# Performance work log

Measured on AMD Instinct MI355X. Metric: run time of the kernel, lower is better.

The kernel has to match this reference:

```python
import jax, jax.numpy as jnp
import numpy as np

N_NODES = 50000
N_EDGES = 800000
D_IN, D_LAT, D_EMB = 512, 256, 64
NEG_SLOPE = 0.2


def segment_softmax(logits, seg, num_segments):
    # numerically stable softmax over variable-size neighborhoods grouped by seg
    m = jax.ops.segment_max(logits, seg, num_segments=num_segments)
    e = jnp.exp(logits - m[seg])
    s = jax.ops.segment_sum(e, seg, num_segments=num_segments)
    return e / s[seg]


def setup_inputs() -> dict:
    key = jax.random.key(0)
    k = jax.random.split(key, 6)
    x = jax.random.normal(k[0], (N_NODES, D_IN), dtype=jnp.float32)
    graph_edges = jax.random.randint(k[1], (2, N_EDGES), 0, N_NODES, dtype=jnp.int32)
    # learned parameters (glorot-ish scaling)
    W1 = jax.random.normal(k[2], (D_IN, D_LAT), dtype=jnp.float32) / np.sqrt(D_IN)
    a1_src = jax.random.normal(k[3], (D_LAT,), dtype=jnp.float32) / np.sqrt(D_LAT)
    a1_dst = jax.random.normal(k[4], (D_LAT,), dtype=jnp.float32) / np.sqrt(D_LAT)
    W2 = jax.random.normal(k[5], (D_LAT, D_EMB), dtype=jnp.float32) / np.sqrt(D_LAT)
    return {"x": x, "W1": W1, "a1_src": a1_src, "a1_dst": a1_dst, "W2": W2,
            "graph_edges": graph_edges}


def reference(x, W1, a1_src, a1_dst, W2, graph_edges):
    src = graph_edges[0]  # message source j
    dst = graph_edges[1]  # aggregation target i
    n = x.shape[0]

    # --- encoder layer 1 (full GAT, heads=1, no bias, no self loops) ---
    h1 = x @ W1                                   # [N, D_LAT]
    als = h1 @ a1_src                             # [N] per-node src logits
    ald = h1 @ a1_dst                             # [N] per-node dst logits
    e1 = jax.nn.leaky_relu(als[src] + ald[dst], NEG_SLOPE)   # [E]
    alpha1 = segment_softmax(e1, dst, n)          # [E]
    agg1 = jax.ops.segment_sum(alpha1[:, None] * h1[src], dst, num_segments=n)
    inter = jax.nn.elu(agg1)                      # [N, D_LAT]

    # --- encoder layer 2 (compute_attention=False -> plain linear) ---
    emb = inter @ W2                              # [N, D_EMB]

    # --- decoder layer 1 (weights tied to W2^T, attention tied to layer1) ---
    h3 = emb @ W2.T                               # [N, D_LAT]
    # tied attention: reuse layer1's per-node logits (als, ald)
    e3 = jax.nn.leaky_relu(als[src] + ald[dst], NEG_SLOPE)
    alpha3 = segment_softmax(e3, dst, n)
    agg3 = jax.ops.segment_sum(alpha3[:, None] * h3[src], dst, num_segments=n)
    dec_inter = jax.nn.elu(agg3)                  # [N, D_LAT]

    # --- decoder layer 2 (compute_attention=False -> plain linear, W1^T) ---
    recon = dec_inter @ W1.T                      # [N, D_IN]
    return emb, recon
```

## Files before the change

### kernel.cpp

```cpp
#include <hip/hip_runtime.h>
#include <math.h>

#define N_NODES 50000
#define N_EDGES 800000
#define D_IN 512
#define D_LAT 256
#define D_EMB 64
#define NEG_SLOPE 0.2f

typedef __attribute__((ext_vector_type(8))) short bf16x8;
typedef __attribute__((ext_vector_type(8))) unsigned short u16x8;
typedef __attribute__((ext_vector_type(4))) float f32x4;

__device__ __forceinline__ ushort f2b(float f) {
  union { float f; unsigned u; } v; v.f = f;
  return (ushort)((v.u + 0x7fffu + ((v.u >> 16) & 1u)) >> 16);
}
__device__ __forceinline__ float b2f(ushort h) {
  union { unsigned u; float f; } v; v.u = ((unsigned)h) << 16;
  return v.f;
}

__device__ __forceinline__ float wave_reduce_sum(float v) {
#pragma unroll
  for (int off = 32; off > 0; off >>= 1) v += __shfl_xor(v, off, 64);
  return v;
}
__device__ __forceinline__ float wave_reduce_max(float v) {
#pragma unroll
  for (int off = 32; off > 0; off >>= 1) v = fmaxf(v, __shfl_xor(v, off, 64));
  return v;
}

template <int BM, int BN, int WR, int WC, int AF32, int WF32, int WBF16,
          int ELU>
__global__ __launch_bounds__(WR * WC * 64) void gemm_mfma(
    const void* __restrict__ Aptr, const ushort* __restrict__ B,
    float* __restrict__ Cf, ushort* __restrict__ Cb, int M, int N, int K) {
  constexpr int BK = 32;
  constexpr int WTM = BM / WR, WTN = BN / WC;
  constexpr int FM = WTM / 16, FN = WTN / 16;
  constexpr int NT = WR * WC * 64;
  constexpr int AIT = (BM * BK * 2) / (NT * 16);
  constexpr int BIT_ = (BN * BK * 2) / (NT * 16);
  __shared__ ushort As[BM][BK];
  __shared__ ushort Bs[BN][BK];
  const int tid = threadIdx.x, lane = tid & 63, wid = tid >> 6;
  const int wr = wid / WC, wc = wid % WC;
  const int bm = blockIdx.y * BM, bn = blockIdx.x * BN;
  f32x4 acc[FM][FN] = {};

  for (int k0 = 0; k0 < K; k0 += BK) {
    if constexpr (AF32) {
      const float* Af = (const float*)Aptr;
#pragma unroll
      for (int it = 0; it < AIT; ++it) {
        int off = it * (NT * 16) + tid * 16;
        int row = off >> 6;
        int ecol = (off & 63) >> 1;
        int grow = bm + row; grow = grow < M ? grow : (M - 1);
        const float* g = Af + (size_t)grow * K + k0 + ecol;
        float4 f0 = *(const float4*)g;
        float4 f1 = *(const float4*)(g + 4);
        u16x8 hb;
        hb[0] = f2b(f0.x); hb[1] = f2b(f0.y); hb[2] = f2b(f0.z); hb[3] = f2b(f0.w);
        hb[4] = f2b(f1.x); hb[5] = f2b(f1.y); hb[6] = f2b(f1.z); hb[7] = f2b(f1.w);
        *(u16x8*)((char*)&As[0][0] + off) = hb;
      }
    } else {
      const ushort* Ab = (const ushort*)Aptr;
#pragma unroll
      for (int it = 0; it < AIT; ++it) {
        int off = it * (NT * 16) + tid * 16;
        int row = off >> 6;
        int grow = bm + row; grow = grow < M ? grow : (M - 1);
        const ushort* g = Ab + (size_t)grow * K + k0 + ((off & 63) >> 1);
        __builtin_amdgcn_global_load_lds(
            (const __attribute__((address_space(1))) void*)g,
            (__attribute__((address_space(3))) void*)((char*)&As[0][0] + off),
            16, 0, 0);
      }
    }
#pragma unroll
    for (int it = 0; it < BIT_; ++it) {
      int off = it * (NT * 16) + tid * 16;
      int row = off >> 6;
      const ushort* g = B + (size_t)(bn + row) * K + k0 + ((off & 63) >> 1);
      __builtin_amdgcn_global_load_lds(
          (const __attribute__((address_space(1))) void*)g,
          (__attribute__((address_space(3))) void*)((char*)&Bs[0][0] + off),
          16, 0, 0);
    }
    __syncthreads();
    const int kb = (lane >> 4) * 8, rl = lane & 15;
    bf16x8 af[FM], bfr[FN];
#pragma unroll
    for (int i = 0; i < FM; ++i)
      af[i] = *(const bf16x8*)&As[wr * WTM + i * 16 + rl][kb];
#pragma unroll
    for (int j = 0; j < FN; ++j)
      bfr[j] = *(const bf16x8*)&Bs[wc * WTN + j * 16 + rl][kb];
#pragma unroll
    for (int i = 0; i < FM; ++i)
#pragma unroll
      for (int j = 0; j < FN; ++j)
        acc[i][j] = __builtin_amdgcn_mfma_f32_16x16x32_bf16(af[i], bfr[j],
                                                            acc[i][j], 0, 0, 0);
    __syncthreads();
  }
  const int cl = lane & 15, rg = (lane >> 4) * 4;
#pragma unroll
  for (int i = 0; i < FM; ++i)
#pragma unroll
    for (int j = 0; j < FN; ++j)
#pragma unroll
      for (int r = 0; r < 4; ++r) {
        int grow = bm + wr * WTM + i * 16 + rg + r;
        if (grow >= M) continue;
        int gcol = bn + wc * WTN + j * 16 + cl;
        float v = acc[i][j][r];
        if (ELU) v = v > 0.f ? v : __expf(v) - 1.f;
        if (WF32) Cf[(size_t)grow * N + gcol] = v;
        if (WBF16) Cb[(size_t)grow * N + gcol] = f2b(v);
      }
}

__global__ __launch_bounds__(256) void conv_weights(
    const float* __restrict__ W1, const float* __restrict__ W2,
    ushort* __restrict__ W1b, ushort* __restrict__ W1tb,
    ushort* __restrict__ W2b, ushort* __restrict__ W2tb) {
  int i = blockIdx.x * blockDim.x + threadIdx.x;
  if (i < D_IN * D_LAT) {
    ushort b = f2b(W1[i]);
    int r = i / D_LAT, c = i % D_LAT;
    W1b[i] = b;
    W1tb[(size_t)c * D_IN + r] = b;
  }
  if (i < D_LAT * D_EMB) {
    ushort b = f2b(W2[i]);
    int r = i / D_EMB, c = i % D_EMB;
    W2b[i] = b;
    W2tb[(size_t)c * D_LAT + r] = b;
  }
}

__global__ __launch_bounds__(256) void node_logits_b(
    const ushort* __restrict__ h1b, const float* __restrict__ a_src,
    const float* __restrict__ a_dst, float* __restrict__ als,
    float* __restrict__ ald) {
  int wave = threadIdx.x >> 6, lane = threadIdx.x & 63;
  int node = blockIdx.x * 4 + wave;
  if (node >= N_NODES) return;
  ushort4 h = *(const ushort4*)(h1b + (size_t)node * D_LAT + lane * 4);
  float4 as4 = *(const float4*)(a_src + lane * 4);
  float4 ad4 = *(const float4*)(a_dst + lane * 4);
  float hx = b2f(h.x), hy = b2f(h.y), hz = b2f(h.z), hw = b2f(h.w);
  float s = hx * as4.x + hy * as4.y + hz * as4.z + hw * as4.w;
  float d = hx * ad4.x + hy * ad4.y + hz * ad4.z + hw * ad4.w;
  s = wave_reduce_sum(s);
  d = wave_reduce_sum(d);
  if (lane == 0) { als[node] = s; ald[node] = d; }
}

__global__ void hist_kernel(const int* __restrict__ dst,
                            int* __restrict__ counts) {
  int e = blockIdx.x * blockDim.x + threadIdx.x;
  if (e < N_EDGES) atomicAdd(&counts[dst[e]], 1);
}

#define SCAN_NBLK ((N_NODES + 511) / 512)

__global__ __launch_bounds__(512) void scan_phase1(
    const int* __restrict__ counts, int* __restrict__ rowptr,
    int* __restrict__ bsum) {
  __shared__ int wsum[9];
  int idx = blockIdx.x * 512 + threadIdx.x;
  int lane = threadIdx.x & 63, wv = threadIdx.x >> 6;
  int c = (idx < N_NODES) ? counts[idx] : 0;
  int v = c;
#pragma unroll
  for (int off = 1; off < 64; off <<= 1) {
    int t = __shfl_up(v, off, 64);
    if (lane >= off) v += t;
  }
  if (lane == 63) wsum[wv] = v;
  __syncthreads();
  if (threadIdx.x == 0) {
    int r = 0;
    for (int i = 0; i < 8; i++) { int t = wsum[i]; wsum[i] = r; r += t; }
    bsum[blockIdx.x] = r;
  }
  __syncthreads();
  if (idx < N_NODES) rowptr[idx] = wsum[wv] + v - c;
}

__global__ __launch_bounds__(128) void scan_phase2(int* __restrict__ bsum) {
  __shared__ int s[128];
  int tid = threadIdx.x;
  int v = (tid < SCAN_NBLK) ? bsum[tid] : 0;
  s[tid] = v;
  __syncthreads();
  for (int off = 1; off < 128; off <<= 1) {
    int t = (tid >= off) ? s[tid - off] : 0;
    __syncthreads();
    s[tid] += t;
    __syncthreads();
  }
  if (tid < SCAN_NBLK) bsum[tid] = s[tid] - v;
}

__global__ __launch_bounds__(512) void scan_phase3(
    int* __restrict__ rowptr, const int* __restrict__ bsum,
    const int* __restrict__ counts) {
  int idx = blockIdx.x * 512 + threadIdx.x;
  if (idx < N_NODES) {
    int r = rowptr[idx] + bsum[blockIdx.x];
    rowptr[idx] = r;
    if (idx == N_NODES - 1) rowptr[N_NODES] = r + counts[idx];
  }
}

__global__ void scatter_kernel(const int* __restrict__ src,
                               const int* __restrict__ dst,
                               const float* __restrict__ als,
                               const float* __restrict__ ald,
                               const int* __restrict__ rowptr,
                               int* __restrict__ fill, int* __restrict__ ssrc,
                               float* __restrict__ slogit) {
  int e = blockIdx.x * blockDim.x + threadIdx.x;
  if (e >= N_EDGES) return;
  int s = src[e], d = dst[e];
  int pos = rowptr[d] + atomicAdd(&fill[d], 1);
  float x = als[s] + ald[d];
  slogit[pos] = (x > 0.f) ? x : NEG_SLOPE * x;
  ssrc[pos] = s;
}

__global__ __launch_bounds__(256) void alpha_kernel(
    const int* __restrict__ rowptr, float* __restrict__ slogit) {
  int wave = threadIdx.x >> 6, lane = threadIdx.x & 63;
  int node = blockIdx.x * 4 + wave;
  if (node >= N_NODES) return;
  int beg = rowptr[node], end = rowptr[node + 1];
  float m = -INFINITY;
  for (int e = beg + lane; e < end; e += 64) m = fmaxf(m, slogit[e]);
  m = wave_reduce_max(m);
  float s = 0.f;
  for (int e = beg + lane; e < end; e += 64) s += __expf(slogit[e] - m);
  s = wave_reduce_sum(s);
  float inv = (s > 0.f) ? 1.f / s : 0.f;
  for (int e = beg + lane; e < end; e += 64)
    slogit[e] = __expf(slogit[e] - m) * inv;
}

__global__ __launch_bounds__(256) void agg_bf16(
    const ushort* __restrict__ feat, const int* __restrict__ rowptr,
    const int* __restrict__ ssrc, const float* __restrict__ alpha,
    ushort* __restrict__ out) {
  int wave = threadIdx.x >> 6, lane = threadIdx.x & 63;
  int node = blockIdx.x * 4 + wave;
  if (node >= N_NODES) return;
  int beg = rowptr[node], end = rowptr[node + 1];
  int half = lane >> 5, hl = lane & 31;
  float acc[8] = {};
  int e = beg + half;
  for (; e + 2 < end; e += 4) {
    float a0 = alpha[e];
    int s0 = ssrc[e];
    float a1 = alpha[e + 2];
    int s1 = ssrc[e + 2];
    u16x8 h0 = *(const u16x8*)(feat + (size_t)s0 * D_LAT + hl * 8);
    u16x8 h1 = *(const u16x8*)(feat + (size_t)s1 * D_LAT + hl * 8);
#pragma unroll
    for (int q = 0; q < 8; q++) acc[q] += a0 * b2f(h0[q]);
#pragma unroll
    for (int q = 0; q < 8; q++) acc[q] += a1 * b2f(h1[q]);
  }
  for (; e < end; e += 2) {
    float a = alpha[e];
    int s = ssrc[e];
    u16x8 h = *(const u16x8*)(feat + (size_t)s * D_LAT + hl * 8);
#pragma unroll
    for (int q = 0; q < 8; q++) acc[q] += a * b2f(h[q]);
  }
#pragma unroll
  for (int q = 0; q < 8; q++) acc[q] += __shfl_xor(acc[q], 32, 64);
  if (half == 0) {
    u16x8 o;
#pragma unroll
    for (int q = 0; q < 8; q++) {
      float v = acc[q];
      o[q] = f2b(v > 0.f ? v : __expf(v) - 1.f);
    }
    *(u16x8*)(out + (size_t)node * D_LAT + hl * 8) = o;
  }
}

__global__ __launch_bounds__(256) void agg_emb(
    const ushort* __restrict__ feat, const int* __restrict__ rowptr,
    const int* __restrict__ ssrc, const float* __restrict__ alpha,
    ushort* __restrict__ out) {
  int wave = threadIdx.x >> 6, lane = threadIdx.x & 63;
  int node = blockIdx.x * 4 + wave;
  if (node >= N_NODES) return;
  int beg = rowptr[node], end = rowptr[node + 1];
  int q = lane >> 4, ql = lane & 15;
  float acc[4] = {};
  for (int e = beg + q; e < end; e += 4) {
    float a = alpha[e];
    int s = ssrc[e];
    ushort4 h = *(const ushort4*)(feat + (size_t)s * D_EMB + ql * 4);
    acc[0] += a * b2f(h.x);
    acc[1] += a * b2f(h.y);
    acc[2] += a * b2f(h.z);
    acc[3] += a * b2f(h.w);
  }
#pragma unroll
  for (int k = 0; k < 4; k++) {
    acc[k] += __shfl_xor(acc[k], 16, 64);
    acc[k] += __shfl_xor(acc[k], 32, 64);
  }
  if (q == 0) {
    ushort4 o;
    o.x = f2b(acc[0]); o.y = f2b(acc[1]); o.z = f2b(acc[2]); o.w = f2b(acc[3]);
    *(ushort4*)(out + (size_t)node * D_EMB + ql * 4) = o;
  }
}

extern "C" void kernel_launch(void* const* d_in, const int* in_sizes, int n_in,
                              void* d_out, int out_size, void* d_ws,
                              size_t ws_size, hipStream_t stream) {
  const float* x = (const float*)d_in[0];
  const float* W1 = (const float*)d_in[1];
  const float* a1s = (const float*)d_in[2];
  const float* a1d = (const float*)d_in[3];
  const float* W2 = (const float*)d_in[4];
  const int* ge = (const int*)d_in[5];
  const int* esrc = ge;
  const int* edst = ge + N_EDGES;

  float* out = (float*)d_out;
  float* emb = out;
  float* recon = out + (size_t)N_NODES * D_EMB;

  char* w = (char*)d_ws;
  ushort* h1b = (ushort*)w;    w += (size_t)N_NODES * D_LAT * 2;
  ushort* interb = (ushort*)w; w += (size_t)N_NODES * D_LAT * 2;
  ushort* embb = (ushort*)w;   w += (size_t)N_NODES * D_EMB * 2;
  ushort* W1b = (ushort*)w;    w += (size_t)D_IN * D_LAT * 2;
  ushort* W1tb = (ushort*)w;   w += (size_t)D_LAT * D_IN * 2;
  ushort* W2b = (ushort*)w;    w += (size_t)D_LAT * D_EMB * 2;
  ushort* W2tb = (ushort*)w;   w += (size_t)D_EMB * D_LAT * 2;
  float* als = (float*)w;      w += (size_t)N_NODES * 4;
  float* ald = (float*)w;      w += (size_t)N_NODES * 4;
  int* counts = (int*)w;       w += (size_t)N_NODES * 4;
  int* rowptr = (int*)w;       w += (size_t)(N_NODES + 4) * 4;
  int* fill = (int*)w;         w += (size_t)N_NODES * 4;
  int* bsum = (int*)w;         w += 128 * 4;
  int* ssrc = (int*)w;         w += (size_t)N_EDGES * 4;
  float* slogit = (float*)w;   w += (size_t)N_EDGES * 4;

  hipMemsetAsync(counts, 0, N_NODES * 4, stream);
  hipMemsetAsync(fill, 0, N_NODES * 4, stream);

  dim3 b256(256), b512(512);
  const int MB = (N_NODES + 127) / 128;

  conv_weights<<<(D_IN * D_LAT + 255) / 256, b256, 0, stream>>>(
      W1, W2, W1b, W1tb, W2b, W2tb);

  gemm_mfma<128, 256, 2, 4, 1, 0, 1, 0><<<dim3(1, MB), b512, 0, stream>>>(
      x, W1tb, (float*)nullptr, h1b, N_NODES, D_LAT, D_IN);
  node_logits_b<<<(N_NODES + 3) / 4, b256, 0, stream>>>(h1b, a1s, a1d, als, ald);
  hist_kernel<<<(N_EDGES + 255) / 256, b256, 0, stream>>>(edst, counts);
  scan_phase1<<<SCAN_NBLK, 512, 0, stream>>>(counts, rowptr, bsum);
  scan_phase2<<<1, 128, 0, stream>>>(bsum);
  scan_phase3<<<SCAN_NBLK, 512, 0, stream>>>(rowptr, bsum, counts);
  scatter_kernel<<<(N_EDGES + 255) / 256, b256, 0, stream>>>(
      esrc, edst, als, ald, rowptr, fill, ssrc, slogit);
  alpha_kernel<<<(N_NODES + 3) / 4, b256, 0, stream>>>(rowptr, slogit);
  agg_bf16<<<(N_NODES + 3) / 4, b256, 0, stream>>>(h1b, rowptr, ssrc, slogit,
                                                   interb);
  gemm_mfma<128, 64, 2, 2, 0, 1, 1, 0><<<dim3(1, MB), b256, 0, stream>>>(
      interb, W2tb, emb, embb, N_NODES, D_EMB, D_LAT);
  ushort* aggEb = interb;
  agg_emb<<<(N_NODES + 3) / 4, b256, 0, stream>>>(embb, rowptr, ssrc, slogit,
                                                  aggEb);
  ushort* decb = h1b;
  gemm_mfma<128, 256, 2, 4, 0, 0, 1, 1><<<dim3(1, MB), b512, 0, stream>>>(
      aggEb, W2b, (float*)nullptr, decb, N_NODES, D_LAT, D_EMB);
  gemm_mfma<128, 256, 2, 4, 0, 1, 0, 0><<<dim3(D_IN / 256, MB), b512, 0, stream>>>(
      decb, W1b, recon, (ushort*)nullptr, N_NODES, D_IN, D_LAT);
}
```

Baseline: 302.5 us.

## Fuse node logits, histogram, scan fixup and softmax into neighboring kernels

Attention logits are now computed in the first GEMM's epilogue from the fp32 accumulators, which removes the node_logits kernel and its re-read of h1. The histogram is folded into the weight-conversion kernel, and the scan's third phase is replaced by adding block offsets on the fly. The softmax normalization moves into the layer-1 aggregation kernel, which writes alpha for reuse by the second aggregation. The two memsets become one. This cuts four kernel launches and several global passes, at the cost of an extra shared-memory atomic epilogue in the GEMM and an extra alpha buffer.

```diff
diff --git a/kernel.cpp b/kernel.cpp
--- a/kernel.cpp
+++ b/kernel.cpp
@@ -33,10 +33,12 @@
 }
 
 template <int BM, int BN, int WR, int WC, int AF32, int WF32, int WBF16,
-          int ELU>
+          int ELU, int LOGIT>
 __global__ __launch_bounds__(WR * WC * 64) void gemm_mfma(
     const void* __restrict__ Aptr, const ushort* __restrict__ B,
-    float* __restrict__ Cf, ushort* __restrict__ Cb, int M, int N, int K) {
+    float* __restrict__ Cf, ushort* __restrict__ Cb, int M, int N, int K,
+    const float* __restrict__ a_src, const float* __restrict__ a_dst,
+    float* __restrict__ als, float* __restrict__ ald) {
   constexpr int BK = 32;
   constexpr int WTM = BM / WR, WTN = BN / WC;
   constexpr int FM = WTM / 16, FN = WTN / 16;
@@ -123,12 +125,51 @@
         if (WF32) Cf[(size_t)grow * N + gcol] = v;
         if (WBF16) Cb[(size_t)grow * N + gcol] = f2b(v);
       }
-}
-
-__global__ __launch_bounds__(256) void conv_weights(
+  if constexpr (LOGIT) {
+    __shared__ float alsP[BM], aldP[BM];
+    for (int t = tid; t < BM; t += NT) { alsP[t] = 0.f; aldP[t] = 0.f; }
+    __syncthreads();
+    float asv[FN], adv[FN];
+#pragma unroll
+    for (int j = 0; j < FN; ++j) {
+      int col = bn + wc * WTN + j * 16 + cl;
+      asv[j] = a_src[col];
+      adv[j] = a_dst[col];
+    }
+#pragma unroll
+    for (int i = 0; i < FM; ++i)
+#pragma unroll
+      for (int r = 0; r < 4; ++r) {
+        float s = 0.f, d = 0.f;
+#pragma unroll
+        for (int j = 0; j < FN; ++j) {
+          s += acc[i][j][r] * asv[j];
+          d += acc[i][j][r] * adv[j];
+        }
+#pragma unroll
+        for (int off = 1; off < 16; off <<= 1) {
+          s += __shfl_xor(s, off, 64);
+          d += __shfl_xor(d, off, 64);
+        }
+        if (cl == 0) {
+          int row = wr * WTM + i * 16 + rg + r;
+          atomicAdd(&alsP[row], s);
+          atomicAdd(&aldP[row], d);
+        }
+      }
+    __syncthreads();
+    for (int t = tid; t < BM; t += NT) {
+      int gr = bm + t;
+      if (gr < M) { als[gr] = alsP[t]; ald[gr] = aldP[t]; }
+    }
+  }
+}
+
+__global__ __launch_bounds__(256) void conv_weights_hist(
     const float* __restrict__ W1, const float* __restrict__ W2,
     ushort* __restrict__ W1b, ushort* __restrict__ W1tb,
-    ushort* __restrict__ W2b, ushort* __restrict__ W2tb) {
+    ushort* __restrict__ W2b, ushort* __restrict__ W2tb,
+    const int* __restrict__ dst, int* __restrict__ counts) {
   int i = blockIdx.x * blockDim.x + threadIdx.x;
   if (i < D_IN * D_LAT) {
     ushort b = f2b(W1[i]);
@@ -142,30 +183,7 @@
     W2b[i] = b;
     W2tb[(size_t)c * D_LAT + r] = b;
   }
-}
-
-__global__ __launch_bounds__(256) void node_logits_b(
-    const ushort* __restrict__ h1b, const float* __restrict__ a_src,
-    const float* __restrict__ a_dst, float* __restrict__ als,
-    float* __restrict__ ald) {
-  int wave = threadIdx.x >> 6, lane = threadIdx.x & 63;
-  int node = blockIdx.x * 4 + wave;
-  if (node >= N_NODES) return;
-  ushort4 h = *(const ushort4*)(h1b + (size_t)node * D_LAT + lane * 4);
-  float4 as4 = *(const float4*)(a_src + lane * 4);
-  float4 ad4 = *(const float4*)(a_dst + lane * 4);
-  float hx = b2f(h.x), hy = b2f(h.y), hz = b2f(h.z), hw = b2f(h.w);
-  float s = hx * as4.x + hy * as4.y + hz * as4.z + hw * as4.w;
-  float d = hx * ad4.x + hy * ad4.y + hz * ad4.z + hw * ad4.w;
-  s = wave_reduce_sum(s);
-  d = wave_reduce_sum(d);
-  if (lane == 0) { als[node] = s; ald[node] = d; }
-}
-
-__global__ void hist_kernel(const int* __restrict__ dst,
-                            int* __restrict__ counts) {
-  int e = blockIdx.x * blockDim.x + threadIdx.x;
-  if (e < N_EDGES) atomicAdd(&counts[dst[e]], 1);
+  if (i < N_EDGES) atomicAdd(&counts[dst[i]], 1);
 }
 
 #define SCAN_NBLK ((N_NODES + 511) / 512)
@@ -209,15 +227,14 @@
   if (tid < SCAN_NBLK) bsum[tid] = s[tid] - v;
 }
 
-__global__ __launch_bounds__(512) void scan_phase3(
-    int* __restrict__ rowptr, const int* __restrict__ bsum,
-    const int* __restrict__ counts) {
-  int idx = blockIdx.x * 512 + threadIdx.x;
-  if (idx < N_NODES) {
-    int r = rowptr[idx] + bsum[blockIdx.x];
-    rowptr[idx] = r;
-    if (idx == N_NODES - 1) rowptr[N_NODES] = r + counts[idx];
-  }
+__device__ __forceinline__ int grp(const int* rowptr, const int* bsum,
+                                   int idx) {
+  return rowptr[idx] + bsum[idx >> 9];
+}
+__device__ __forceinline__ int grp_end(const int* rowptr, const int* bsum,
+                                       int node) {
+  return (node + 1 < N_NODES) ? rowptr[node + 1] + bsum[(node + 1) >> 9]
+                              : N_EDGES;
 }
 
 __global__ void scatter_kernel(const int* __restrict__ src,
@@ -225,23 +242,27 @@
                                const float* __restrict__ als,
                                const float* __restrict__ ald,
                                const int* __restrict__ rowptr,
+                               const int* __restrict__ bsum,
                                int* __restrict__ fill, int* __restrict__ ssrc,
                                float* __restrict__ slogit) {
   int e = blockIdx.x * blockDim.x + threadIdx.x;
   if (e >= N_EDGES) return;
   int s = src[e], d = dst[e];
-  int pos = rowptr[d] + atomicAdd(&fill[d], 1);
+  int pos = grp(rowptr, bsum, d) + atomicAdd(&fill[d], 1);
   float x = als[s] + ald[d];
   slogit[pos] = (x > 0.f) ? x : NEG_SLOPE * x;
   ssrc[pos] = s;
 }
 
-__global__ __launch_bounds__(256) void alpha_kernel(
-    const int* __restrict__ rowptr, float* __restrict__ slogit) {
+__global__ __launch_bounds__(256) void agg_bf16_sm(
+    const ushort* __restrict__ feat, const int* __restrict__ rowptr,
+    const int* __restrict__ bsum, const int* __restrict__ ssrc,
+    const float* __restrict__ slogit, float* __restrict__ alphaOut,
+    ushort* __restrict__ out) {
   int wave = threadIdx.x >> 6, lane = threadIdx.x & 63;
   int node = blockIdx.x * 4 + wave;
   if (node >= N_NODES) return;
-  int beg = rowptr[node], end = rowptr[node + 1];
+  int beg = grp(rowptr, bsum, node), end = grp_end(rowptr, bsum, node);
   float m = -INFINITY;
   for (int e = beg + lane; e < end; e += 64) m = fmaxf(m, slogit[e]);
   m = wave_reduce_max(m);
@@ -249,26 +270,15 @@
   for (int e = beg + lane; e < end; e += 64) s += __expf(slogit[e] - m);
   s = wave_reduce_sum(s);
   float inv = (s > 0.f) ? 1.f / s : 0.f;
-  for (int e = beg + lane; e < end; e += 64)
-    slogit[e] = __expf(slogit[e] - m) * inv;
-}
-
-__global__ __launch_bounds__(256) void agg_bf16(
-    const ushort* __restrict__ feat, const int* __restrict__ rowptr,
-    const int* __restrict__ ssrc, const float* __restrict__ alpha,
-    ushort* __restrict__ out) {
-  int wave = threadIdx.x >> 6, lane = threadIdx.x & 63;
-  int node = blockIdx.x * 4 + wave;
-  if (node >= N_NODES) return;
-  int beg = rowptr[node], end = rowptr[node + 1];
   int half = lane >> 5, hl = lane & 31;
   float acc[8] = {};
   int e = beg + half;
   for (; e + 2 < end; e += 4) {
-    float a0 = alpha[e];
+    float a0 = __expf(slogit[e] - m) * inv;
     int s0 = ssrc[e];
-    float a1 = alpha[e + 2];
+    float a1 = __expf(slogit[e + 2] - m) * inv;
     int s1 = ssrc[e + 2];
+    if (hl == 0) { alphaOut[e] = a0; alphaOut[e + 2] = a1; }
     u16x8 h0 = *(const u16x8*)(feat + (size_t)s0 * D_LAT + hl * 8);
     u16x8 h1 = *(const u16x8*)(feat + (size_t)s1 * D_LAT + hl * 8);
 #pragma unroll
@@ -277,9 +287,10 @@
     for (int q = 0; q < 8; q++) acc[q] += a1 * b2f(h1[q]);
   }
   for (; e < end; e += 2) {
-    float a = alpha[e];
-    int s = ssrc[e];
-    u16x8 h = *(const u16x8*)(feat + (size_t)s * D_LAT + hl * 8);
+    float a = __expf(slogit[e] - m) * inv;
+    int s2 = ssrc[e];
+    if (hl == 0) alphaOut[e] = a;
+    u16x8 h = *(const u16x8*)(feat + (size_t)s2 * D_LAT + hl * 8);
 #pragma unroll
     for (int q = 0; q < 8; q++) acc[q] += a * b2f(h[q]);
   }
@@ -298,12 +309,12 @@
 
 __global__ __launch_bounds__(256) void agg_emb(
     const ushort* __restrict__ feat, const int* __restrict__ rowptr,
-    const int* __restrict__ ssrc, const float* __restrict__ alpha,
-    ushort* __restrict__ out) {
+    const int* __restrict__ bsum, const int* __restrict__ ssrc,
+    const float* __restrict__ alpha, ushort* __restrict__ out) {
   int wave = threadIdx.x >> 6, lane = threadIdx.x & 63;
   int node = blockIdx.x * 4 + wave;
   if (node >= N_NODES) return;
-  int beg = rowptr[node], end = rowptr[node + 1];
+  int beg = grp(rowptr, bsum, node), end = grp_end(rowptr, bsum, node);
   int q = lane >> 4, ql = lane & 15;
   float acc[4] = {};
   for (int e = beg + q; e < end; e += 4) {
@@ -354,41 +365,41 @@
   float* als = (float*)w;      w += (size_t)N_NODES * 4;
   float* ald = (float*)w;      w += (size_t)N_NODES * 4;
   int* counts = (int*)w;       w += (size_t)N_NODES * 4;
+  int* fill = (int*)w;         w += (size_t)N_NODES * 4;
   int* rowptr = (int*)w;       w += (size_t)(N_NODES + 4) * 4;
-  int* fill = (int*)w;         w += (size_t)N_NODES * 4;
   int* bsum = (int*)w;         w += 128 * 4;
   int* ssrc = (int*)w;         w += (size_t)N_EDGES * 4;
   float* slogit = (float*)w;   w += (size_t)N_EDGES * 4;
-
-  hipMemsetAsync(counts, 0, N_NODES * 4, stream);
-  hipMemsetAsync(fill, 0, N_NODES * 4, stream);
+  float* alphaO = (float*)w;   w += (size_t)N_EDGES * 4;
+
+  hipMemsetAsync(counts, 0, (size_t)N_NODES * 8, stream);
 
   dim3 b256(256), b512(512);
   const int MB = (N_NODES + 127) / 128;
 
-  conv_weights<<<(D_IN * D_LAT + 255) / 256, b256, 0, stream>>>(
-      W1, W2, W1b, W1tb, W2b, W2tb);
-
-  gemm_mfma<128, 256, 2, 4, 1, 0, 1, 0><<<dim3(1, MB), b512, 0, stream>>>(
-      x, W1tb, (float*)nullptr, h1b, N_NODES, D_LAT, D_IN);
-  node_logits_b<<<(N_NODES + 3) / 4, b256, 0, stream>>>(h1b, a1s, a1d, als, ald);
-  hist_kernel<<<(N_EDGES + 255) / 256, b256, 0, stream>>>(edst, counts);
+  conv_weights_hist<<<(N_EDGES + 255) / 256, b256, 0, stream>>>(
+      W1, W2, W1b, W1tb, W2b, W2tb, edst, counts);
+
+  gemm_mfma<128, 256, 2, 4, 1, 0, 1, 0, 1><<<dim3(1, MB), b512, 0, stream>>>(
+      x, W1tb, (float*)nullptr, h1b, N_NODES, D_LAT, D_IN, a1s, a1d, als, ald);
   scan_phase1<<<SCAN_NBLK, 512, 0, stream>>>(counts, rowptr, bsum);
   scan_phase2<<<1, 128, 0, stream>>>(bsum);
-  scan_phase3<<<SCAN_NBLK, 512, 0, stream>>>(rowptr, bsum, counts);
   scatter_kernel<<<(N_EDGES + 255) / 256, b256, 0, stream>>>(
-      esrc, edst, als, ald, rowptr, fill, ssrc, slogit);
-  alpha_kernel<<<(N_NODES + 3) / 4, b256, 0, stream>>>(rowptr, slogit);
-  agg_bf16<<<(N_NODES + 3) / 4, b256, 0, stream>>>(h1b, rowptr, ssrc, slogit,
-                                                   interb);
-  gemm_mfma<128, 64, 2, 2, 0, 1, 1, 0><<<dim3(1, MB), b256, 0, stream>>>(
-      interb, W2tb, emb, embb, N_NODES, D_EMB, D_LAT);
+      esrc, edst, als, ald, rowptr, bsum, fill, ssrc, slogit);
+  agg_bf16_sm<<<(N_NODES + 3) / 4, b256, 0, stream>>>(
+      h1b, rowptr, bsum, ssrc, slogit, alphaO, interb);
+  gemm_mfma<128, 64, 2, 2, 0, 1, 1, 0, 0><<<dim3(1, MB), b256, 0, stream>>>(
+      interb, W2tb, emb, embb, N_NODES, D_EMB, D_LAT, nullptr, nullptr,
+      nullptr, nullptr);
   ushort* aggEb = interb;
-  agg_emb<<<(N_NODES + 3) / 4, b256, 0, stream>>>(embb, rowptr, ssrc, slogit,
-                                                  aggEb);
+  agg_emb<<<(N_NODES + 3) / 4, b256, 0, stream>>>(embb, rowptr, bsum, ssrc,
+                                                  alphaO, aggEb);
   ushort* decb = h1b;
-  gemm_mfma<128, 256, 2, 4, 0, 0, 1, 1><<<dim3(1, MB), b512, 0, stream>>>(
-      aggEb, W2b, (float*)nullptr, decb, N_NODES, D_LAT, D_EMB);
-  gemm_mfma<128, 256, 2, 4, 0, 1, 0, 0><<<dim3(D_IN / 256, MB), b512, 0, stream>>>(
-      decb, W1b, recon, (ushort*)nullptr, N_NODES, D_IN, D_LAT);
-}
+  gemm_mfma<128, 256, 2, 4, 0, 0, 1, 1, 0><<<dim3(1, MB), b512, 0, stream>>>(
+      aggEb, W2b, (float*)nullptr, decb, N_NODES, D_LAT, D_EMB, nullptr,
+      nullptr, nullptr, nullptr);
+  gemm_mfma<128, 256, 2, 4, 0, 1, 0, 0, 0><<<dim3(D_IN / 256, MB), b512, 0,
+                                              stream>>>(
+      decb, W1b, recon, (ushort*)nullptr, N_NODES, D_IN, D_LAT, nullptr,
+      nullptr, nullptr, nullptr);
+}
```

Result: faster. 291.1 us (-3.8%).
